# Performance work log

Hardware: AMD Instinct MI355X
Metric: run time of the kernel (lower is better)

The kernel has to match this reference:

```python
import jax, jax.numpy as jnp
import numpy as np

B = 131072
T = 30
H = 150
STATIC_D = 50


def _expm_sym2x2(S):
    """Closed-form V diag(exp(e)) V^T for symmetric (B,2,2) S.

    Equals exp(tr/2) * (cosh(d) I + sinh(d)/d * (S - tr/2 I)), d = sqrt(((a-c)/2)^2 + b^2).
    This is exactly what torch.symeig + exp(e) reconstruction computes.
    """
    a = S[:, 0, 0]
    b = S[:, 0, 1]
    c = S[:, 1, 1]
    half_tr = 0.5 * (a + c)
    half_diff = 0.5 * (a - c)
    disc = jnp.sqrt(half_diff * half_diff + b * b)
    d = jnp.maximum(disc, 1e-12)
    sinhc = jnp.sinh(d) / d
    coshd = jnp.cosh(disc)
    scale = jnp.exp(half_tr)
    m00 = scale * (coshd + sinhc * half_diff)
    m11 = scale * (coshd - sinhc * half_diff)
    m01 = scale * (sinhc * b)
    row0 = jnp.stack([m00, m01], axis=-1)
    row1 = jnp.stack([m01, m11], axis=-1)
    return jnp.stack([row0, row1], axis=-2)  # (B,2,2)


def setup_inputs() -> dict:
    key = jax.random.key(0)
    ks = jax.random.split(key, 12)
    s = lambda fan_in: 1.0 / np.sqrt(fan_in)
    inp = {
        "static": jax.random.normal(ks[0], (B, STATIC_D), jnp.float32),
        "init_velocity": jax.random.normal(ks[1], (B, 2), jnp.float32),
        "init_position": jax.random.normal(ks[2], (B, 2), jnp.float32),
        "z": jax.random.normal(ks[3], (T, B, 2), jnp.float32),
        # GRU params (PyTorch layout: gates [r, z, n] stacked along dim 0)
        "W_ih": jax.random.uniform(ks[4], (3 * H, T * 2), jnp.float32, -s(H), s(H)),
        "W_hh": jax.random.uniform(ks[5], (3 * H, H), jnp.float32, -s(H), s(H)),
        "b_ih": jax.random.uniform(ks[6], (3 * H,), jnp.float32, -s(H), s(H)),
        "b_hh": jax.random.uniform(ks[7], (3 * H,), jnp.float32, -s(H), s(H)),
        # MLP params
        "W1": jax.random.uniform(ks[8], (50, H + STATIC_D), jnp.float32, -s(H + STATIC_D), s(H + STATIC_D)),
        "b1": jax.random.uniform(ks[9], (50,), jnp.float32, -s(H + STATIC_D), s(H + STATIC_D)),
        "W2": jax.random.uniform(ks[10], (6, 50), jnp.float32, -s(50), s(50)),
        "b2": jax.random.uniform(ks[11], (6,), jnp.float32, -s(50), s(50)),
    }
    return inp


def reference(static, init_velocity, init_position, z, W_ih, W_hh, b_ih, b_hh, W1, b1, W2, b2):
    batch = static.shape[0]
    h0 = jnp.zeros((batch, H), jnp.float32)
    xbuf0 = jnp.zeros((batch, T, 2), jnp.float32)

    def step(carry, inp):
        h, xbuf, dx, x_prev = carry
        i, zi = inp
        x_flat = xbuf.reshape(batch, T * 2)
        # GRU cell (single layer, seq_len 1)
        gi = x_flat @ W_ih.T + b_ih
        gh = h @ W_hh.T + b_hh
        ir, iz, inn = jnp.split(gi, 3, axis=1)
        hr, hz, hn = jnp.split(gh, 3, axis=1)
        r = jax.nn.sigmoid(ir + hr)
        zg = jax.nn.sigmoid(iz + hz)
        n = jnp.tanh(inn + r * hn)
        h_new = (1.0 - zg) * n + zg * h
        # MLP on [dynamic_encoding, static]
        ds = jnp.concatenate([h_new, static], axis=1)
        o = jax.nn.softplus(ds @ W1.T + b1)
        o = jax.nn.softplus(o @ W2.T + b2)
        mu_hat = o[:, :2]
        sig_hat = o[:, 2:].reshape(batch, 2, 2)
        S = sig_hat + jnp.swapaxes(sig_hat, 1, 2)
        sigma = _expm_sym2x2(S)
        mu = x_prev + dx + mu_hat
        x_ = jnp.einsum('bij,bj->bi', sigma, zi) + mu
        xbuf = jax.lax.dynamic_update_slice(xbuf, x_[:, None, :], (0, i, 0))
        return (h_new, xbuf, x_ - x_prev, x_), (mu, sigma, x_)

    _, (mu, sigma, x) = jax.lax.scan(
        step, (h0, xbuf0, init_velocity, init_position), (jnp.arange(T), z)
    )
    return mu, sigma, x  # (30,B,2), (30,B,2,2), (30,B,2)
```

## Files before the change

### kernel.cpp

```cpp
#include <hip/hip_runtime.h>
#include <math.h>


typedef _Float16 f16;
typedef _Float16 f16x8 __attribute__((ext_vector_type(8)));
typedef float    f32x4 __attribute__((ext_vector_type(4)));

constexpr int BTOT = 131072;
constexpr int TSTEPS = 30;
constexpr int H  = 150;
constexpr int SD = 50;
constexpr int BT = 16;
constexpr int NT = 512;
constexpr int NBLK = 256;
constexpr int NGRP = BTOT / (NBLK * BT);

constexpr int HP = 160;
constexpr int NP = 480;
constexpr int AHS = 232;

constexpr int WS_WIHT  = 0;
constexpr int WS_BFRAG = 115200;

constexpr int SIG_OFF = TSTEPS * BTOT * 2;
constexpr int X_OFF   = SIG_OFF + TSTEPS * BTOT * 4;

__device__ __forceinline__ float fexp(float x)  { return __builtin_amdgcn_exp2f(x * 1.44269504f); }
__device__ __forceinline__ float sigm(float x)  { return __builtin_amdgcn_rcpf(1.f + __builtin_amdgcn_exp2f(-1.44269504f * x)); }
__device__ __forceinline__ float tanh_(float x) { return fmaf(-2.f, __builtin_amdgcn_rcpf(1.f + __builtin_amdgcn_exp2f(2.88539008f * x)), 1.f); }
__device__ __forceinline__ float softplus_(float v) {
    float e = __builtin_amdgcn_exp2f(-1.44269504f * fabsf(v));
    return fmaxf(v, 0.f) + 0.69314718f * __builtin_amdgcn_logf(1.f + e);
}

__global__ void r2p2_prep(const float* __restrict__ Wih, float* __restrict__ ws) {
    int id = blockIdx.x * 256 + threadIdx.x;
    if (id >= TSTEPS * NP) return;
    int s = id / NP, tp = id - s * NP;
    int g = tp / HP, off = tp - g * HP;
    float2 v = make_float2(0.f, 0.f);
    if (off < H) {
        const float* row = Wih + (g * H + off) * (2 * TSTEPS);
        v.x = row[2 * s];
        v.y = row[2 * s + 1];
    }
    ((float2*)ws)[id] = v;
}

__global__ void r2p2_prep2(const float* __restrict__ Whh, f16* __restrict__ wsB) {
    int id = blockIdx.x * 256 + threadIdx.x;
    if (id >= 9600) return;
    int lane = id & 63, rest = id >> 6;
    int kk = rest % 5, kg = rest / 5;
    int g = kg % 3, k = kg / 3;
    int lr = lane & 15, lq = lane >> 4;
    int nr = k * 16 + lr;
    f16x8 v;
    #pragma unroll
    for (int j = 0; j < 8; ++j) {
        int cc = kk * 32 + lq * 8 + j;
        float x = (nr < H && cc < H) ? Whh[(g * H + nr) * H + cc] : 0.f;
        v[j] = (f16)x;
    }
    *(f16x8*)(wsB + (size_t)id * 8) = v;
}

__global__ __launch_bounds__(NT, 2) void r2p2_main(
    const float* __restrict__ statp, const float* __restrict__ initv,
    const float* __restrict__ initp, const float* __restrict__ zp,
    const float* __restrict__ bih,   const float* __restrict__ bhh,
    const float* __restrict__ W1,    const float* __restrict__ b1,
    const float* __restrict__ W2,    const float* __restrict__ b2,
    const float* __restrict__ wihT,  const f16* __restrict__ wsB,
    float* __restrict__ out)
{
    __shared__ __align__(16) f16   sA[BT * AHS];
    __shared__ __align__(16) f16   sW1[64 * AHS];
    __shared__ __align__(16) f16   sO1[16 * 64];
    __shared__ __align__(16) f16   sW2[16 * 64];
    __shared__ __align__(16) float sO2[16 * 8];
    __shared__ __align__(16) float sZ[TSTEPS * 32];
    __shared__ __align__(16) float sXC[32];
    __shared__ __align__(16) float sXP[32];
    __shared__ __align__(16) float sDX[32];

    const int t  = threadIdx.x;
    const int w  = t >> 6;
    const int l  = t & 63;
    const int lr = l & 15;
    const int lq = l >> 4;

    int ntr = 0, tr0 = 0;
    if (w < 4)       { ntr = 1; tr0 = w; }
    else if (w >= 5) { ntr = 2; tr0 = 4 + (w - 5) * 2; }

    for (int i = t; i < BT * AHS / 2; i += NT) ((unsigned*)sA)[i] = 0u;
    for (int i = t; i < 64 * AHS; i += NT) {
        int r = i / AHS, k = i - r * AHS;
        float v = 0.f;
        if (r < SD && k < 224) {
            if (k < H) v = W1[r * 200 + k];
            else if (k >= HP && k < HP + SD) v = W1[r * 200 + H + (k - HP)];
        }
        sW1[i] = (f16)v;
    }
    for (int i = t; i < 16 * 64; i += NT) {
        int r = i / 64, k = i - r * 64;
        sW2[i] = (f16)((r < 6 && k < SD) ? W2[r * SD + k] : 0.f);
        sO1[i] = (f16)0.f;
    }

    f16x8 bfrag[2][3][5];
    #pragma unroll
    for (int tt = 0; tt < 2; ++tt) {
        if (tt < ntr) {
            int k = tr0 + tt;
            #pragma unroll
            for (int g = 0; g < 3; ++g)
                #pragma unroll
                for (int kk = 0; kk < 5; ++kk)
                    bfrag[tt][g][kk] = *(const f16x8*)(wsB + ((size_t)((k * 3 + g) * 5 + kk) * 64 + l) * 8);
        }
    }
    float cR[2], cZ[2], cNi[2], cNh[2];
    #pragma unroll
    for (int tt = 0; tt < 2; ++tt) {
        cR[tt] = cZ[tt] = cNi[tt] = cNh[tt] = 0.f;
        if (tt < ntr) {
            int u = (tr0 + tt) * 16 + lr;
            if (u < H) {
                cR[tt]  = bih[u]         + bhh[u];
                cZ[tt]  = bih[H + u]     + bhh[H + u];
                cNi[tt] = bih[2 * H + u];
                cNh[tt] = bhh[2 * H + u];
            }
        }
    }
    const int   p3col  = w * 16 + lr;
    const float b1reg  = (w < 4 && p3col < SD) ? b1[p3col] : 0.f;
    const float b2reg  = (lr < 6) ? b2[lr] : 0.f;

    float hreg[2][4];
    f32x4 acc[2][3];
    f32x4 gi[2][3];

    for (int grp = 0; grp < NGRP; ++grp) {
        const int bg0 = (grp * NBLK + blockIdx.x) * BT;
        __syncthreads();
        for (int i = t; i < BT * SD; i += NT) {
            int b = i / SD, k = i - b * SD;
            sA[b * AHS + HP + k] = (f16)statp[(bg0 + b) * SD + k];
        }
        for (int i = t; i < TSTEPS * 32; i += NT)
            sZ[i] = zp[((size_t)(i >> 5) * BTOT + bg0) * 2 + (i & 31)];
        if (t < 2 * BT) {
            sXP[t] = initp[bg0 * 2 + t];
            sDX[t] = initv[bg0 * 2 + t];
        }
        #pragma unroll
        for (int tt = 0; tt < 2; ++tt) {
            #pragma unroll
            for (int j = 0; j < 4; ++j) hreg[tt][j] = 0.f;
            #pragma unroll
            for (int g = 0; g < 3; ++g) acc[tt][g] = (f32x4){0.f, 0.f, 0.f, 0.f};
            gi[tt][0] = (f32x4){cR[tt],  cR[tt],  cR[tt],  cR[tt]};
            gi[tt][1] = (f32x4){cZ[tt],  cZ[tt],  cZ[tt],  cZ[tt]};
            gi[tt][2] = (f32x4){cNi[tt], cNi[tt], cNi[tt], cNi[tt]};
        }
        __syncthreads();

        for (int s = 0; s < TSTEPS; ++s) {
            if (ntr > 0) {
                if (s > 0) {
                    f32x4 xa = *(const f32x4*)&sXC[lq * 8];
                    f32x4 xb = *(const f32x4*)&sXC[lq * 8 + 4];
                    const float* wT = wihT + (size_t)(s - 1) * (NP * 2);
                    #pragma unroll
                    for (int tt = 0; tt < 2; ++tt) {
                        if (tt < ntr) {
                            int u = (tr0 + tt) * 16 + lr;
                            #pragma unroll
                            for (int g = 0; g < 3; ++g) {
                                float2 wv = *(const float2*)(wT + (g * HP + u) * 2);
                                gi[tt][g][0] = fmaf(wv.x, xa[0], fmaf(wv.y, xa[1], gi[tt][g][0]));
                                gi[tt][g][1] = fmaf(wv.x, xa[2], fmaf(wv.y, xa[3], gi[tt][g][1]));
                                gi[tt][g][2] = fmaf(wv.x, xb[0], fmaf(wv.y, xb[1], gi[tt][g][2]));
                                gi[tt][g][3] = fmaf(wv.x, xb[2], fmaf(wv.y, xb[3], gi[tt][g][3]));
                            }
                        }
                    }
                }
                #pragma unroll
                for (int tt = 0; tt < 2; ++tt) {
                    if (tt < ntr) {
                        int u = (tr0 + tt) * 16 + lr;
                        #pragma unroll
                        for (int j = 0; j < 4; ++j) {
                            float r  = sigm(acc[tt][0][j] + gi[tt][0][j]);
                            float zg = sigm(acc[tt][1][j] + gi[tt][1][j]);
                            float n  = tanh_(gi[tt][2][j] + r * (acc[tt][2][j] + cNh[tt]));
                            float hv = (1.f - zg) * n + zg * hreg[tt][j];
                            hreg[tt][j] = hv;
                            if (u < H) sA[(lq * 4 + j) * AHS + u] = (f16)hv;
                        }
                    }
                }
            }
            __syncthreads();

            if (w < 4) {
                f32x4 a3 = (f32x4){0.f, 0.f, 0.f, 0.f};
                #pragma unroll
                for (int kk = 0; kk < 7; ++kk) {
                    f16x8 av = *(const f16x8*)(sA  + lr    * AHS + kk * 32 + lq * 8);
                    f16x8 bv = *(const f16x8*)(sW1 + p3col * AHS + kk * 32 + lq * 8);
                    a3 = __builtin_amdgcn_mfma_f32_16x16x32_f16(av, bv, a3, 0, 0, 0);
                }
                if (p3col < SD) {
                    #pragma unroll
                    for (int j = 0; j < 4; ++j)
                        sO1[(lq * 4 + j) * 64 + p3col] = (f16)softplus_(a3[j] + b1reg);
                }
            } else if (w >= 5 && s + 1 < TSTEPS) {
                f16x8 af[5];
                #pragma unroll
                for (int kk = 0; kk < 5; ++kk)
                    af[kk] = *(const f16x8*)(sA + lr * AHS + kk * 32 + lq * 8);
                #pragma unroll
                for (int tt = 0; tt < 2; ++tt) {
                    #pragma unroll
                    for (int g = 0; g < 3; ++g) {
                        acc[tt][g] = (f32x4){0.f, 0.f, 0.f, 0.f};
                        #pragma unroll
                        for (int kk = 0; kk < 5; ++kk)
                            acc[tt][g] = __builtin_amdgcn_mfma_f32_16x16x32_f16(af[kk], bfrag[tt][g][kk], acc[tt][g], 0, 0, 0);
                    }
                }
            }
            __syncthreads();

            if (w == 4) {
                f32x4 a4 = (f32x4){0.f, 0.f, 0.f, 0.f};
                #pragma unroll
                for (int kk = 0; kk < 2; ++kk) {
                    f16x8 av = *(const f16x8*)(sO1 + lr * 64 + kk * 32 + lq * 8);
                    f16x8 bv = *(const f16x8*)(sW2 + lr * 64 + kk * 32 + lq * 8);
                    a4 = __builtin_amdgcn_mfma_f32_16x16x32_f16(av, bv, a4, 0, 0, 0);
                }
                if (lr < 6) {
                    #pragma unroll
                    for (int j = 0; j < 4; ++j)
                        sO2[(lq * 4 + j) * 8 + lr] = softplus_(a4[j] + b2reg);
                }
                asm volatile("s_waitcnt lgkmcnt(0)" ::: "memory");
                if (l < BT) {
                    const int b  = l;
                    const int bg = bg0 + b;
                    f32x4  v0 = *(const f32x4*)&sO2[b * 8];
                    float2 v1 = *(const float2*)&sO2[b * 8 + 4];
                    float mh0 = v0[0], mh1 = v0[1];
                    float a = 2.f * v0[2], bb2 = v0[3] + v1.x, c = 2.f * v1.y;
                    float htr = 0.5f * (a + c), hdf = 0.5f * (a - c);
                    float disc = sqrtf(hdf * hdf + bb2 * bb2);
                    float d = fmaxf(disc, 1e-12f);
                    float ep = fexp(d), em = fexp(-d);
                    float sinhc = (0.5f * (ep - em)) * __builtin_amdgcn_rcpf(d);
                    float coshd = 0.5f * (ep + em);
                    float scale = fexp(htr);
                    float m00 = scale * (coshd + sinhc * hdf);
                    float m11 = scale * (coshd - sinhc * hdf);
                    float m01 = scale * (sinhc * bb2);

                    float z0 = sZ[s * 32 + 2 * b], z1 = sZ[s * 32 + 2 * b + 1];
                    float xp0 = sXP[2 * b], xp1 = sXP[2 * b + 1];
                    float mu0 = xp0 + sDX[2 * b]     + mh0;
                    float mu1 = xp1 + sDX[2 * b + 1] + mh1;
                    float x0 = fmaf(m00, z0, fmaf(m01, z1, mu0));
                    float x1 = fmaf(m01, z0, fmaf(m11, z1, mu1));

                    const size_t oi = (size_t)s * BTOT + bg;
                    *(float2*)(out + oi * 2) = make_float2(mu0, mu1);
                    *(float4*)(out + SIG_OFF + oi * 4) = make_float4(m00, m01, m01, m11);
                    *(float2*)(out + X_OFF + oi * 2) = make_float2(x0, x1);

                    sXC[2 * b] = x0;       sXC[2 * b + 1] = x1;
                    sDX[2 * b] = x0 - xp0; sDX[2 * b + 1] = x1 - xp1;
                    sXP[2 * b] = x0;       sXP[2 * b + 1] = x1;
                }
            } else if (w < 4 && s + 1 < TSTEPS) {
                f16x8 af[5];
                #pragma unroll
                for (int kk = 0; kk < 5; ++kk)
                    af[kk] = *(const f16x8*)(sA + lr * AHS + kk * 32 + lq * 8);
                #pragma unroll
                for (int g = 0; g < 3; ++g) {
                    acc[0][g] = (f32x4){0.f, 0.f, 0.f, 0.f};
                    #pragma unroll
                    for (int kk = 0; kk < 5; ++kk)
                        acc[0][g] = __builtin_amdgcn_mfma_f32_16x16x32_f16(af[kk], bfrag[0][g][kk], acc[0][g], 0, 0, 0);
                }
            }
            __syncthreads();
        }
    }
}

extern "C" void kernel_launch(void* const* d_in, const int* in_sizes, int n_in,
                              void* d_out, int out_size, void* d_ws, size_t ws_size,
                              hipStream_t stream) {
    const float* statp = (const float*)d_in[0];
    const float* initv = (const float*)d_in[1];
    const float* initp = (const float*)d_in[2];
    const float* zp    = (const float*)d_in[3];
    const float* Wih   = (const float*)d_in[4];
    const float* Whh   = (const float*)d_in[5];
    const float* bih   = (const float*)d_in[6];
    const float* bhh   = (const float*)d_in[7];
    const float* W1    = (const float*)d_in[8];
    const float* b1    = (const float*)d_in[9];
    const float* W2    = (const float*)d_in[10];
    const float* b2    = (const float*)d_in[11];
    float* out  = (float*)d_out;
    float* wihT = (float*)((char*)d_ws + WS_WIHT);
    f16*   wsB  = (f16*)  ((char*)d_ws + WS_BFRAG);

    r2p2_prep <<<(TSTEPS * NP + 255) / 256, 256, 0, stream>>>(Wih, wihT);
    r2p2_prep2<<<(9600 + 255) / 256, 256, 0, stream>>>(Whh, wsB);
    r2p2_main<<<NBLK, NT, 0, stream>>>(
        statp, initv, initp, zp, bih, bhh, W1, b1, W2, b2, wihT, wsB, out);
}
```

Before: 2.240 ms.

## Stage outputs in LDS, prefetch input weights a step ahead, pad O1 stride

Per-step global stores of mu, sigma and x by a single wave are replaced with writes to an LDS staging buffer. After all 30 steps the buffer is flushed by 480 threads in parallel, which takes global stores off the serial recurrence critical path. The W_ih weights for the next step are loaded into registers after the barrier, overlapping the global load with the MLP phase. The sO1/sW2 row stride is padded from 64 to 72 to reduce LDS bank conflicts. This costs about 15 KB of extra LDS and more registers, which could affect the two-blocks-per-CU occupancy.

```diff
diff --git a/kernel.cpp b/kernel.cpp
--- a/kernel.cpp
+++ b/kernel.cpp
@@ -18,6 +18,7 @@
 constexpr int HP = 160;
 constexpr int NP = 480;
 constexpr int AHS = 232;
+constexpr int O1S = 72;
 
 constexpr int WS_WIHT  = 0;
 constexpr int WS_BFRAG = 115200;
@@ -76,10 +77,11 @@
 {
     __shared__ __align__(16) f16   sA[BT * AHS];
     __shared__ __align__(16) f16   sW1[64 * AHS];
-    __shared__ __align__(16) f16   sO1[16 * 64];
-    __shared__ __align__(16) f16   sW2[16 * 64];
+    __shared__ __align__(16) f16   sO1[16 * O1S];
+    __shared__ __align__(16) f16   sW2[16 * O1S];
     __shared__ __align__(16) float sO2[16 * 8];
     __shared__ __align__(16) float sZ[TSTEPS * 32];
+    __shared__ __align__(16) float sOUT[TSTEPS * 16 * 8];
     __shared__ __align__(16) float sXC[32];
     __shared__ __align__(16) float sXP[32];
     __shared__ __align__(16) float sDX[32];
@@ -104,8 +106,8 @@
         }
         sW1[i] = (f16)v;
     }
-    for (int i = t; i < 16 * 64; i += NT) {
-        int r = i / 64, k = i - r * 64;
+    for (int i = t; i < 16 * O1S; i += NT) {
+        int r = i / O1S, k = i - r * O1S;
         sW2[i] = (f16)((r < 6 && k < SD) ? W2[r * SD + k] : 0.f);
         sO1[i] = (f16)0.f;
     }
@@ -143,6 +145,7 @@
     float hreg[2][4];
     f32x4 acc[2][3];
     f32x4 gi[2][3];
+    float2 wvp[2][3];
 
     for (int grp = 0; grp < NGRP; ++grp) {
         const int bg0 = (grp * NBLK + blockIdx.x) * BT;
@@ -174,14 +177,12 @@
                 if (s > 0) {
                     f32x4 xa = *(const f32x4*)&sXC[lq * 8];
                     f32x4 xb = *(const f32x4*)&sXC[lq * 8 + 4];
-                    const float* wT = wihT + (size_t)(s - 1) * (NP * 2);
                     #pragma unroll
                     for (int tt = 0; tt < 2; ++tt) {
                         if (tt < ntr) {
-                            int u = (tr0 + tt) * 16 + lr;
                             #pragma unroll
                             for (int g = 0; g < 3; ++g) {
-                                float2 wv = *(const float2*)(wT + (g * HP + u) * 2);
+                                float2 wv = wvp[tt][g];
                                 gi[tt][g][0] = fmaf(wv.x, xa[0], fmaf(wv.y, xa[1], gi[tt][g][0]));
                                 gi[tt][g][1] = fmaf(wv.x, xa[2], fmaf(wv.y, xa[3], gi[tt][g][1]));
                                 gi[tt][g][2] = fmaf(wv.x, xb[0], fmaf(wv.y, xb[1], gi[tt][g][2]));
@@ -208,6 +209,19 @@
             }
             __syncthreads();
 
+            if (ntr > 0 && s + 1 < TSTEPS) {
+                const float* wT = wihT + (size_t)s * (NP * 2);
+                #pragma unroll
+                for (int tt = 0; tt < 2; ++tt) {
+                    if (tt < ntr) {
+                        int u = (tr0 + tt) * 16 + lr;
+                        #pragma unroll
+                        for (int g = 0; g < 3; ++g)
+                            wvp[tt][g] = *(const float2*)(wT + (g * HP + u) * 2);
+                    }
+                }
+            }
+
             if (w < 4) {
                 f32x4 a3 = (f32x4){0.f, 0.f, 0.f, 0.f};
                 #pragma unroll
@@ -219,7 +233,7 @@
                 if (p3col < SD) {
                     #pragma unroll
                     for (int j = 0; j < 4; ++j)
-                        sO1[(lq * 4 + j) * 64 + p3col] = (f16)softplus_(a3[j] + b1reg);
+                        sO1[(lq * 4 + j) * O1S + p3col] = (f16)softplus_(a3[j] + b1reg);
                 }
             } else if (w >= 5 && s + 1 < TSTEPS) {
                 f16x8 af[5];
@@ -243,8 +257,8 @@
                 f32x4 a4 = (f32x4){0.f, 0.f, 0.f, 0.f};
                 #pragma unroll
                 for (int kk = 0; kk < 2; ++kk) {
-                    f16x8 av = *(const f16x8*)(sO1 + lr * 64 + kk * 32 + lq * 8);
-                    f16x8 bv = *(const f16x8*)(sW2 + lr * 64 + kk * 32 + lq * 8);
+                    f16x8 av = *(const f16x8*)(sO1 + lr * O1S + kk * 32 + lq * 8);
+                    f16x8 bv = *(const f16x8*)(sW2 + lr * O1S + kk * 32 + lq * 8);
                     a4 = __builtin_amdgcn_mfma_f32_16x16x32_f16(av, bv, a4, 0, 0, 0);
                 }
                 if (lr < 6) {
@@ -254,8 +268,7 @@
                 }
                 asm volatile("s_waitcnt lgkmcnt(0)" ::: "memory");
                 if (l < BT) {
-                    const int b  = l;
-                    const int bg = bg0 + b;
+                    const int b = l;
                     f32x4  v0 = *(const f32x4*)&sO2[b * 8];
                     float2 v1 = *(const float2*)&sO2[b * 8 + 4];
                     float mh0 = v0[0], mh1 = v0[1];
@@ -278,10 +291,9 @@
                     float x0 = fmaf(m00, z0, fmaf(m01, z1, mu0));
                     float x1 = fmaf(m01, z0, fmaf(m11, z1, mu1));
 
-                    const size_t oi = (size_t)s * BTOT + bg;
-                    *(float2*)(out + oi * 2) = make_float2(mu0, mu1);
-                    *(float4*)(out + SIG_OFF + oi * 4) = make_float4(m00, m01, m01, m11);
-                    *(float2*)(out + X_OFF + oi * 2) = make_float2(x0, x1);
+                    float* st = &sOUT[(s * 16 + b) * 8];
+                    *(float4*)(st)     = make_float4(mu0, mu1, m00, m01);
+                    *(float4*)(st + 4) = make_float4(m11, x0, x1, 0.f);
 
                     sXC[2 * b] = x0;       sXC[2 * b + 1] = x1;
                     sDX[2 * b] = x0 - xp0; sDX[2 * b + 1] = x1 - xp1;
@@ -301,6 +313,15 @@
                 }
             }
             __syncthreads();
+        }
+
+        if (t < TSTEPS * 16) {
+            int s = t >> 4, b = t & 15;
+            const float* src = &sOUT[(s * 16 + b) * 8];
+            const size_t oi = (size_t)s * BTOT + bg0 + b;
+            *(float2*)(out + oi * 2)           = make_float2(src[0], src[1]);
+            *(float4*)(out + SIG_OFF + oi * 4) = make_float4(src[2], src[3], src[3], src[4]);
+            *(float2*)(out + X_OFF + oi * 2)   = make_float2(src[5], src[6]);
         }
     }
 }
```

New measurement: 2.191 ms. 1.02x faster.
